# Optimization experiments

Hardware: AMD Instinct MI355X
Metric: run time of the kernel (lower is better)

The kernel has to match this reference:

```python
import jax, jax.numpy as jnp
import numpy as np

B, S, D, MD = 4, 4096, 1024, 512
SCALE = 0.02  # init scale for weights


def _layernorm(x, g, b, eps=1e-5):
    m = jnp.mean(x, axis=-1, keepdims=True)
    v = jnp.mean((x - m) ** 2, axis=-1, keepdims=True)
    return (x - m) * jax.lax.rsqrt(v + eps) * g + b


def _mem_mlp(h, W0, W1):
    # MemoryMLP depth=2: linear -> gelu -> linear (no biases)
    return jax.nn.gelu(h @ W0) @ W1


def _assoc_scan(gates, inputs):
    # state_t = g_t * state_{t-1} + in_t, over the seq axis (axis=1)
    def step(state, gi):
        g, i = gi
        s = g * state + i
        return s, s
    init = jnp.zeros_like(inputs[:, 0])
    _, out = jax.lax.scan(step, init, (jnp.moveaxis(gates, 1, 0), jnp.moveaxis(inputs, 1, 0)))
    return jnp.moveaxis(out, 1, 0)


def setup_inputs() -> dict:
    key = jax.random.key(0)
    ks = jax.random.split(key, 10)
    return {
        "x": jax.random.normal(ks[0], (B, S, D), jnp.float32),
        "Wd": jax.random.normal(ks[1], (D, MD), jnp.float32) * SCALE,
        "bd": jnp.zeros((MD,), jnp.float32),
        "Wu": jax.random.normal(ks[2], (MD, D), jnp.float32) * SCALE,
        "bu": jnp.zeros((D,), jnp.float32),
        "Wq": jax.random.normal(ks[3], (MD, MD), jnp.float32) * SCALE,
        "bq": jnp.zeros((MD,), jnp.float32),
        "Wk": jax.random.normal(ks[4], (MD, MD), jnp.float32) * SCALE,
        "bk": jnp.zeros((MD,), jnp.float32),
        "Wv": jax.random.normal(ks[5], (MD, MD), jnp.float32) * SCALE,
        "bv": jnp.zeros((MD,), jnp.float32),
        "q_gamma": jnp.ones((MD,), jnp.float32),
        "q_beta": jnp.zeros((MD,), jnp.float32),
        "k_gamma": jnp.ones((MD,), jnp.float32),
        "k_beta": jnp.zeros((MD,), jnp.float32),
        "W0": jax.random.normal(ks[6], (MD, MD), jnp.float32) * SCALE,
        "W1": jax.random.normal(ks[7], (MD, MD), jnp.float32) * SCALE,
        "adaptive_lr": jnp.full((1,), 0.01, jnp.float32),
        "forget_factor": jnp.full((1,), 0.1, jnp.float32),
    }


def reference(x, Wd, bd, Wu, bu, Wq, bq, Wk, bk, Wv, bv,
              q_gamma, q_beta, k_gamma, k_beta, W0, W1,
              adaptive_lr, forget_factor):
    h = x @ Wd + bd                                   # [B,S,MD] down_proj
    q = _layernorm(h @ Wq + bq, q_gamma, q_beta)      # q_norm(to_queries)
    k = _layernorm(h @ Wk + bk, k_gamma, k_beta)      # k_norm(to_keys)
    v = h @ Wv + bv                                   # to_values
    retrieved = _mem_mlp(q, W0, W1)                   # memory read
    pred = _mem_mlp(k, W0, W1)                        # memory store pred
    # per-token surprise: MSE over feature dim
    surprise = jnp.mean((pred - v) ** 2, axis=-1, keepdims=True)  # [B,S,1]
    gate_val = 1.0 - jax.nn.sigmoid(forget_factor)[0]
    gates = jnp.full((B, S, 1), 1.0, jnp.float32) * gate_val
    inputs = adaptive_lr[0] * surprise * v            # surprise-weighted write
    scanned = _assoc_scan(gates, inputs)              # sequential recurrence
    out = (retrieved + scanned) @ Wu + bu             # up_proj
    return out
```

## Files before the change

kernel.cpp:

```cpp
#include <hip/hip_runtime.h>
#include <hip/hip_bf16.h>
#include <math.h>

#define B_    4
#define S_    4096
#define DD    1024
#define MD    512
#define NTOK  16384
#define CHUNK 128
#define NCH   32

typedef unsigned short u16;
typedef __attribute__((ext_vector_type(8))) short short8;
typedef __attribute__((ext_vector_type(4))) float f32x4;

__device__ __forceinline__ float bf2f(u16 u) {
    unsigned int x = ((unsigned int)u) << 16;
    return __builtin_bit_cast(float, x);
}
__device__ __forceinline__ u16 f2bf(float f) {
    unsigned int x = __builtin_bit_cast(unsigned int, f);
    unsigned int lsb = (x >> 16) & 1u;
    x += 0x7fffu + lsb;
    return (u16)(x >> 16);
}
__device__ __forceinline__ float gelu_f(float x) {
    float x3 = x * x * x;
    return 0.5f * x * (1.0f + tanhf(0.7978845608028654f * (x + 0.044715f * x3)));
}
__device__ __forceinline__ float gate_from_ff(const float* ff) {
    return 1.0f - 1.0f / (1.0f + expf(-ff[0]));
}

#define GLDS(gp, lp) __builtin_amdgcn_global_load_lds( \
    (const __attribute__((address_space(1))) void*)(gp), \
    (__attribute__((address_space(3))) void*)(lp), 16, 0, 0)

template<int EPI, int HB, int OUTBF>
__global__ __launch_bounds__(256) void gemm_bf16_k(
    const u16* __restrict__ A, const u16* __restrict__ BT,
    const float* __restrict__ bias, void* __restrict__ C,
    int N, int K, int M)
{
    __shared__ __align__(16) u16 Al[2][128 * 32];
    __shared__ __align__(16) u16 Bl[2][128 * 32];
    const int tid = threadIdx.x;
    const int w = tid >> 6, l = tid & 63;
    const int rowBase = blockIdx.y * 128, colBase = blockIdx.x * 128;
    const int wm = (w >> 1) * 64, wn = (w & 1) * 64;

    const int srow = l >> 2;
    const int skoff = (l & 3) * 8;
    const u16* Ag0 = A  + (size_t)(rowBase + w * 16 + srow) * K + skoff;
    const u16* Ag1 = A  + (size_t)(rowBase + (w + 4) * 16 + srow) * K + skoff;
    const u16* Bg0 = BT + (size_t)(colBase + w * 16 + srow) * K + skoff;
    const u16* Bg1 = BT + (size_t)(colBase + (w + 4) * 16 + srow) * K + skoff;

    f32x4 acc[4][4];
#pragma unroll
    for (int i = 0; i < 4; ++i)
#pragma unroll
        for (int j = 0; j < 4; ++j) acc[i][j] = (f32x4){0.f, 0.f, 0.f, 0.f};

    const int KT = K >> 5;
    GLDS(Ag0, &Al[0][(w * 16) * 32]);
    GLDS(Ag1, &Al[0][((w + 4) * 16) * 32]);
    GLDS(Bg0, &Bl[0][(w * 16) * 32]);
    GLDS(Bg1, &Bl[0][((w + 4) * 16) * 32]);
    __syncthreads();

    const int lr = l & 15;
    const int goff = (l >> 4) * 8;
    int cur = 0;
    for (int kt = 0; kt < KT; ++kt) {
        if (kt + 1 < KT) {
            const size_t ko = (size_t)(kt + 1) << 5;
            GLDS(Ag0 + ko, &Al[cur ^ 1][(w * 16) * 32]);
            GLDS(Ag1 + ko, &Al[cur ^ 1][((w + 4) * 16) * 32]);
            GLDS(Bg0 + ko, &Bl[cur ^ 1][(w * 16) * 32]);
            GLDS(Bg1 + ko, &Bl[cur ^ 1][((w + 4) * 16) * 32]);
        }
        short8 af[4], bfr[4];
#pragma unroll
        for (int m = 0; m < 4; ++m)
            af[m] = *(const short8*)&Al[cur][(wm + m * 16 + lr) * 32 + goff];
#pragma unroll
        for (int n = 0; n < 4; ++n)
            bfr[n] = *(const short8*)&Bl[cur][(wn + n * 16 + lr) * 32 + goff];
#pragma unroll
        for (int m = 0; m < 4; ++m)
#pragma unroll
            for (int n = 0; n < 4; ++n)
                acc[m][n] = __builtin_amdgcn_mfma_f32_16x16x32_bf16(af[m], bfr[n], acc[m][n], 0, 0, 0);
        __syncthreads();
        cur ^= 1;
    }

    const int g4 = (l >> 4) * 4;
#pragma unroll
    for (int n = 0; n < 4; ++n) {
        const int col = colBase + wn + n * 16 + lr;
        const float bj = HB ? bias[col] : 0.0f;
#pragma unroll
        for (int m = 0; m < 4; ++m) {
            const int row0 = rowBase + wm + m * 16 + g4;
#pragma unroll
            for (int q = 0; q < 4; ++q) {
                float vv = acc[m][n][q] + bj;
                if (EPI == 1) vv = gelu_f(vv);
                if (OUTBF) ((u16*)C)[(size_t)(row0 + q) * M + col] = f2bf(vv);
                else       ((float*)C)[(size_t)(row0 + q) * M + col] = vv;
            }
        }
    }
}

__global__ __launch_bounds__(256) void cvt_bf16_k(const float* __restrict__ in,
                                                  u16* __restrict__ out, int n)
{
    size_t i = ((size_t)blockIdx.x * 256 + threadIdx.x) * 8;
    if (i + 8 > (size_t)n) return;
    float4 a = *(const float4*)(in + i);
    float4 b = *(const float4*)(in + i + 4);
    short8 o;
    o[0] = (short)f2bf(a.x); o[1] = (short)f2bf(a.y);
    o[2] = (short)f2bf(a.z); o[3] = (short)f2bf(a.w);
    o[4] = (short)f2bf(b.x); o[5] = (short)f2bf(b.y);
    o[6] = (short)f2bf(b.z); o[7] = (short)f2bf(b.w);
    *(short8*)(out + i) = o;
}

__global__ __launch_bounds__(256) void wtrans_k(const float* __restrict__ W,
                                                u16* __restrict__ WT, int K, int M)
{
    __shared__ float t[32][33];
    const int tx = threadIdx.x, ty = threadIdx.y;
    const int m0 = blockIdx.x * 32, k0 = blockIdx.y * 32;
#pragma unroll
    for (int i = 0; i < 4; ++i)
        t[ty + i * 8][tx] = W[(size_t)(k0 + ty + i * 8) * M + m0 + tx];
    __syncthreads();
#pragma unroll
    for (int i = 0; i < 4; ++i)
        WT[(size_t)(m0 + ty + i * 8) * K + k0 + tx] = f2bf(t[tx][ty + i * 8]);
}

__global__ __launch_bounds__(256) void wtrans5_k(
    const float* __restrict__ Wa, const float* __restrict__ Wb,
    const float* __restrict__ Wc, const float* __restrict__ Wd_,
    const float* __restrict__ We,
    u16* __restrict__ Ta, u16* __restrict__ Tb, u16* __restrict__ Tc,
    u16* __restrict__ Td, u16* __restrict__ Te)
{
    __shared__ float t[32][33];
    const float* W; u16* T;
    switch (blockIdx.z) {
        case 0: W = Wa; T = Ta; break;
        case 1: W = Wb; T = Tb; break;
        case 2: W = Wc; T = Tc; break;
        case 3: W = Wd_; T = Td; break;
        default: W = We; T = Te; break;
    }
    const int tx = threadIdx.x, ty = threadIdx.y;
    const int m0 = blockIdx.x * 32, k0 = blockIdx.y * 32;
#pragma unroll
    for (int i = 0; i < 4; ++i)
        t[ty + i * 8][tx] = W[(size_t)(k0 + ty + i * 8) * 512 + m0 + tx];
    __syncthreads();
#pragma unroll
    for (int i = 0; i < 4; ++i)
        T[(size_t)(m0 + ty + i * 8) * 512 + k0 + tx] = f2bf(t[tx][ty + i * 8]);
}

__global__ __launch_bounds__(256) void ln_k(const float* __restrict__ X,
                                            u16* __restrict__ Y,
                                            const float* __restrict__ g,
                                            const float* __restrict__ b)
{
    const int row = blockIdx.x, tid = threadIdx.x;
    const float* x = X + (size_t)row * MD;
    float v0 = x[tid], v1 = x[tid + 256];
    float s = v0 + v1, q = v0 * v0 + v1 * v1;
#pragma unroll
    for (int off = 32; off > 0; off >>= 1) {
        s += __shfl_down(s, off);
        q += __shfl_down(q, off);
    }
    __shared__ float redS[4], redQ[4];
    __shared__ float s_mean, s_rstd;
    const int lane = tid & 63, w = tid >> 6;
    if (lane == 0) { redS[w] = s; redQ[w] = q; }
    __syncthreads();
    if (tid == 0) {
        float S = redS[0] + redS[1] + redS[2] + redS[3];
        float Q = redQ[0] + redQ[1] + redQ[2] + redQ[3];
        float m = S * (1.f / 512.f);
        float var = Q * (1.f / 512.f) - m * m;
        s_mean = m; s_rstd = rsqrtf(var + 1e-5f);
    }
    __syncthreads();
    const float m = s_mean, rs = s_rstd;
    u16* y = Y + (size_t)row * MD;
    y[tid]       = f2bf((v0 - m) * rs * g[tid]       + b[tid]);
    y[tid + 256] = f2bf((v1 - m) * rs * g[tid + 256] + b[tid + 256]);
}

__global__ __launch_bounds__(256) void surprise_k(const u16* __restrict__ pred,
                                                  u16* __restrict__ v,
                                                  const float* __restrict__ lr_p)
{
    const int row = blockIdx.x, tid = threadIdx.x;
    const u16* pp = pred + (size_t)row * MD;
    u16* vp = v + (size_t)row * MD;
    float p0 = bf2f(pp[tid]), p1 = bf2f(pp[tid + 256]);
    float v0 = bf2f(vp[tid]), v1 = bf2f(vp[tid + 256]);
    float d0 = p0 - v0, d1 = p1 - v1;
    float q = d0 * d0 + d1 * d1;
#pragma unroll
    for (int off = 32; off > 0; off >>= 1) q += __shfl_down(q, off);
    __shared__ float redQ[4];
    __shared__ float s_coef;
    const int lane = tid & 63, w = tid >> 6;
    if (lane == 0) redQ[w] = q;
    __syncthreads();
    if (tid == 0) {
        float Q = redQ[0] + redQ[1] + redQ[2] + redQ[3];
        s_coef = lr_p[0] * (Q * (1.f / 512.f));
    }
    __syncthreads();
    const float c = s_coef;
    vp[tid]       = f2bf(c * v0);
    vp[tid + 256] = f2bf(c * v1);
}

__global__ __launch_bounds__(256) void scan1_k(u16* __restrict__ io,
                                               const float* __restrict__ ff,
                                               float* __restrict__ carry)
{
    const int idx = blockIdx.x * blockDim.x + threadIdx.x;
    const int d = idx & (MD - 1);
    const int c = (idx >> 9) & (NCH - 1);
    const int b = idx >> 14;
    const float g = gate_from_ff(ff);
    u16* p = io + ((size_t)(b * S_ + c * CHUNK)) * MD + d;
    float s = 0.f;
#pragma unroll 4
    for (int t = 0; t < CHUNK; ++t) {
        s = fmaf(g, s, bf2f(p[(size_t)t * MD]));
        p[(size_t)t * MD] = f2bf(s);
    }
    carry[((size_t)b * NCH + c) * MD + d] = s;
}

__global__ __launch_bounds__(256) void scan2_k(const float* __restrict__ carry,
                                               const float* __restrict__ ff,
                                               float* __restrict__ Sin)
{
    const int idx = blockIdx.x * blockDim.x + threadIdx.x;
    const int d = idx & (MD - 1);
    const int b = idx >> 9;
    const float g = gate_from_ff(ff);
    const float gL = powf(g, (float)CHUNK);
    float p = 0.f;
    for (int c = 0; c < NCH; ++c) {
        Sin[((size_t)b * NCH + c) * MD + d] = p;
        p = carry[((size_t)b * NCH + c) * MD + d] + gL * p;
    }
}

__global__ __launch_bounds__(256) void scan3_k(const u16* __restrict__ loc,
                                               const float* __restrict__ Sin,
                                               const float* __restrict__ retr,
                                               const float* __restrict__ ff,
                                               u16* __restrict__ fin)
{
    const size_t idx = (size_t)blockIdx.x * blockDim.x + threadIdx.x;
    const int d = (int)(idx & (MD - 1));
    const int t = (int)((idx >> 9) & (S_ - 1));
    const int b = (int)(idx >> 21);
    const int c = t >> 7, tl = t & (CHUNK - 1);
    const float g = gate_from_ff(ff);
    const float f = exp2f((float)(tl + 1) * log2f(g));
    float v = bf2f(loc[idx]) + f * Sin[((size_t)b * NCH + c) * MD + d] + retr[idx];
    fin[idx] = f2bf(v);
}

extern "C" void kernel_launch(void* const* d_in, const int* in_sizes, int n_in,
                              void* d_out, int out_size, void* d_ws, size_t ws_size,
                              hipStream_t stream) {
    const float* x   = (const float*)d_in[0];
    const float* Wd  = (const float*)d_in[1];
    const float* bd  = (const float*)d_in[2];
    const float* Wu  = (const float*)d_in[3];
    const float* bu  = (const float*)d_in[4];
    const float* Wq  = (const float*)d_in[5];
    const float* bq  = (const float*)d_in[6];
    const float* Wk  = (const float*)d_in[7];
    const float* bk  = (const float*)d_in[8];
    const float* Wv  = (const float*)d_in[9];
    const float* bv  = (const float*)d_in[10];
    const float* qg  = (const float*)d_in[11];
    const float* qb  = (const float*)d_in[12];
    const float* kg  = (const float*)d_in[13];
    const float* kb  = (const float*)d_in[14];
    const float* W0  = (const float*)d_in[15];
    const float* W1  = (const float*)d_in[16];
    const float* lr  = (const float*)d_in[17];
    const float* ff  = (const float*)d_in[18];
    float* out = (float*)d_out;

    u16* wdT = (u16*)d_ws;
    u16* wqT = wdT + 512 * 1024;
    u16* wkT = wqT + 512 * 512;
    u16* wvT = wkT + 512 * 512;
    u16* w0T = wvT + 512 * 512;
    u16* w1T = w0T + 512 * 512;
    u16* wuT = w1T + 512 * 512;
    u16* xb  = wuT + 1024 * 512;
    u16* b1  = xb;
    u16* b2  = xb + (size_t)NTOK * MD;
    u16* hb  = xb + (size_t)NTOK * DD;
    u16* b3  = hb;
    float* P   = (float*)(hb + (size_t)NTOK * MD);
    u16* VB    = (u16*)(P + (size_t)NTOK * MD);
    float* carry = (float*)(VB + (size_t)NTOK * MD);
    float* Sin   = carry + B_ * NCH * MD;

    dim3 blk(256);
    dim3 t32(32, 8);

    cvt_bf16_k<<<(NTOK * DD) / (256 * 8), blk, 0, stream>>>(x, xb, NTOK * DD);
    wtrans_k<<<dim3(512 / 32, 1024 / 32), t32, 0, stream>>>(Wd, wdT, 1024, 512);
    wtrans5_k<<<dim3(16, 16, 5), t32, 0, stream>>>(Wq, Wk, Wv, W0, W1,
                                                   wqT, wkT, wvT, w0T, w1T);
    wtrans_k<<<dim3(1024 / 32, 512 / 32), t32, 0, stream>>>(Wu, wuT, 512, 1024);

    gemm_bf16_k<0, 1, 1><<<dim3(4, 128), blk, 0, stream>>>(xb, wdT, bd, hb, NTOK, 1024, 512);
    gemm_bf16_k<0, 1, 0><<<dim3(4, 128), blk, 0, stream>>>(hb, wqT, bq, P, NTOK, 512, 512);
    ln_k<<<NTOK, blk, 0, stream>>>(P, b1, qg, qb);
    gemm_bf16_k<0, 1, 0><<<dim3(4, 128), blk, 0, stream>>>(hb, wkT, bk, P, NTOK, 512, 512);
    ln_k<<<NTOK, blk, 0, stream>>>(P, b2, kg, kb);
    gemm_bf16_k<0, 1, 1><<<dim3(4, 128), blk, 0, stream>>>(hb, wvT, bv, VB, NTOK, 512, 512);
    gemm_bf16_k<1, 0, 1><<<dim3(4, 128), blk, 0, stream>>>(b1, w0T, nullptr, b3, NTOK, 512, 512);
    gemm_bf16_k<0, 0, 0><<<dim3(4, 128), blk, 0, stream>>>(b3, w1T, nullptr, P, NTOK, 512, 512);
    gemm_bf16_k<1, 0, 1><<<dim3(4, 128), blk, 0, stream>>>(b2, w0T, nullptr, b3, NTOK, 512, 512);
    gemm_bf16_k<0, 0, 1><<<dim3(4, 128), blk, 0, stream>>>(b3, w1T, nullptr, b1, NTOK, 512, 512);
    surprise_k<<<NTOK, blk, 0, stream>>>(b1, VB, lr);
    scan1_k<<<(B_ * NCH * MD) / 256, blk, 0, stream>>>(VB, ff, carry);
    scan2_k<<<(B_ * MD) / 256, blk, 0, stream>>>(carry, ff, Sin);
    scan3_k<<<(NTOK * MD) / 256, blk, 0, stream>>>(VB, Sin, P, ff, b2);
    gemm_bf16_k<0, 1, 0><<<dim3(8, 128), blk, 0, stream>>>(b2, wuT, bu, out, NTOK, 512, 1024);
}
```

Before: 304.5 us.

## Fuse QKV projections and batch memory-MLP GEMMs; vectorize scan and packed bf16 stores

Concatenates Wq/Wk/Wv into one GEMM that writes bf16 outputs into three segmented buffers, and runs LayerNorm for q and k in place in a single launch. The two memory-MLP passes share one GEMM pair over 2*NTOK rows (q and k buffers are contiguous). The surprise coefficient is folded into the scan instead of rewriting V, scan kernels use 4-wide vector loads with smaller chunks, and the GEMM epilogue packs bf16 pairs via lane shuffles. The down-projection uses a narrower 64-column tile for more blocks. This reduces launches and intermediate fp32 round trips at the cost of more template complexity and bf16 rounding of pre-LN activations.

```diff
diff --git a/kernel.cpp b/kernel.cpp
--- a/kernel.cpp
+++ b/kernel.cpp
@@ -7,20 +7,22 @@
 #define DD    1024
 #define MD    512
 #define NTOK  16384
-#define CHUNK 128
-#define NCH   32
+#define CHUNK 32
+#define NCH   128
 
 typedef unsigned short u16;
+typedef unsigned int u32;
 typedef __attribute__((ext_vector_type(8))) short short8;
 typedef __attribute__((ext_vector_type(4))) float f32x4;
+typedef __attribute__((ext_vector_type(4))) unsigned short us4;
 
 __device__ __forceinline__ float bf2f(u16 u) {
-    unsigned int x = ((unsigned int)u) << 16;
+    u32 x = ((u32)u) << 16;
     return __builtin_bit_cast(float, x);
 }
 __device__ __forceinline__ u16 f2bf(float f) {
-    unsigned int x = __builtin_bit_cast(unsigned int, f);
-    unsigned int lsb = (x >> 16) & 1u;
+    u32 x = __builtin_bit_cast(u32, f);
+    u32 lsb = (x >> 16) & 1u;
     x += 0x7fffu + lsb;
     return (u16)(x >> 16);
 }
@@ -36,37 +38,40 @@
     (const __attribute__((address_space(1))) void*)(gp), \
     (__attribute__((address_space(3))) void*)(lp), 16, 0, 0)
 
-template<int EPI, int HB, int OUTBF>
+template<int NF, int EPI, int HB, int OUTBF, int SEG>
 __global__ __launch_bounds__(256) void gemm_bf16_k(
     const u16* __restrict__ A, const u16* __restrict__ BT,
-    const float* __restrict__ bias, void* __restrict__ C,
-    int N, int K, int M)
-{
+    const float* __restrict__ bias0, const float* __restrict__ bias1,
+    const float* __restrict__ bias2,
+    void* __restrict__ out0, void* __restrict__ out1, void* __restrict__ out2,
+    int N, int K, int M, int OM)
+{
+    constexpr int TN = 32 * NF;
     __shared__ __align__(16) u16 Al[2][128 * 32];
-    __shared__ __align__(16) u16 Bl[2][128 * 32];
+    __shared__ __align__(16) u16 Bl[2][TN * 32];
     const int tid = threadIdx.x;
     const int w = tid >> 6, l = tid & 63;
-    const int rowBase = blockIdx.y * 128, colBase = blockIdx.x * 128;
-    const int wm = (w >> 1) * 64, wn = (w & 1) * 64;
+    const int rowBase = blockIdx.y * 128, colBase = blockIdx.x * TN;
+    const int wm = (w >> 1) * 64, wn = (w & 1) * 16 * NF;
 
     const int srow = l >> 2;
     const int skoff = (l & 3) * 8;
-    const u16* Ag0 = A  + (size_t)(rowBase + w * 16 + srow) * K + skoff;
-    const u16* Ag1 = A  + (size_t)(rowBase + (w + 4) * 16 + srow) * K + skoff;
+    const u16* Ag0 = A + (size_t)(rowBase + w * 16 + srow) * K + skoff;
+    const u16* Ag1 = A + (size_t)(rowBase + (w + 4) * 16 + srow) * K + skoff;
     const u16* Bg0 = BT + (size_t)(colBase + w * 16 + srow) * K + skoff;
-    const u16* Bg1 = BT + (size_t)(colBase + (w + 4) * 16 + srow) * K + skoff;
-
-    f32x4 acc[4][4];
-#pragma unroll
-    for (int i = 0; i < 4; ++i)
-#pragma unroll
-        for (int j = 0; j < 4; ++j) acc[i][j] = (f32x4){0.f, 0.f, 0.f, 0.f};
+    const u16* Bg1 = (NF == 4) ? BT + (size_t)(colBase + (w + 4) * 16 + srow) * K + skoff : nullptr;
+
+    f32x4 acc[4][NF];
+#pragma unroll
+    for (int i = 0; i < 4; ++i)
+#pragma unroll
+        for (int j = 0; j < NF; ++j) acc[i][j] = (f32x4){0.f, 0.f, 0.f, 0.f};
 
     const int KT = K >> 5;
     GLDS(Ag0, &Al[0][(w * 16) * 32]);
     GLDS(Ag1, &Al[0][((w + 4) * 16) * 32]);
     GLDS(Bg0, &Bl[0][(w * 16) * 32]);
-    GLDS(Bg1, &Bl[0][((w + 4) * 16) * 32]);
+    if (NF == 4) GLDS(Bg1, &Bl[0][((w + 4) * 16) * 32]);
     __syncthreads();
 
     const int lr = l & 15;
@@ -78,38 +83,62 @@
             GLDS(Ag0 + ko, &Al[cur ^ 1][(w * 16) * 32]);
             GLDS(Ag1 + ko, &Al[cur ^ 1][((w + 4) * 16) * 32]);
             GLDS(Bg0 + ko, &Bl[cur ^ 1][(w * 16) * 32]);
-            GLDS(Bg1 + ko, &Bl[cur ^ 1][((w + 4) * 16) * 32]);
+            if (NF == 4) GLDS(Bg1 + ko, &Bl[cur ^ 1][((w + 4) * 16) * 32]);
         }
-        short8 af[4], bfr[4];
+        short8 af[4], bfr[NF];
 #pragma unroll
         for (int m = 0; m < 4; ++m)
             af[m] = *(const short8*)&Al[cur][(wm + m * 16 + lr) * 32 + goff];
 #pragma unroll
-        for (int n = 0; n < 4; ++n)
+        for (int n = 0; n < NF; ++n)
             bfr[n] = *(const short8*)&Bl[cur][(wn + n * 16 + lr) * 32 + goff];
 #pragma unroll
         for (int m = 0; m < 4; ++m)
 #pragma unroll
-            for (int n = 0; n < 4; ++n)
+            for (int n = 0; n < NF; ++n)
                 acc[m][n] = __builtin_amdgcn_mfma_f32_16x16x32_bf16(af[m], bfr[n], acc[m][n], 0, 0, 0);
         __syncthreads();
         cur ^= 1;
     }
 
     const int g4 = (l >> 4) * 4;
-#pragma unroll
-    for (int n = 0; n < 4; ++n) {
+    const bool odd = l & 1;
+#pragma unroll
+    for (int n = 0; n < NF; ++n) {
         const int col = colBase + wn + n * 16 + lr;
-        const float bj = HB ? bias[col] : 0.0f;
+        const int seg = SEG ? (col >> 9) : 0;
+        const int lcol = SEG ? (col - (seg << 9)) : col;
+        const float* bp = (seg == 0) ? bias0 : (seg == 1) ? bias1 : bias2;
+        void* outp = (seg == 0) ? out0 : (seg == 1) ? out1 : out2;
+        const float bj = HB ? bp[lcol] : 0.0f;
 #pragma unroll
         for (int m = 0; m < 4; ++m) {
             const int row0 = rowBase + wm + m * 16 + g4;
+            float vq[4];
 #pragma unroll
             for (int q = 0; q < 4; ++q) {
                 float vv = acc[m][n][q] + bj;
                 if (EPI == 1) vv = gelu_f(vv);
-                if (OUTBF) ((u16*)C)[(size_t)(row0 + q) * M + col] = f2bf(vv);
-                else       ((float*)C)[(size_t)(row0 + q) * M + col] = vv;
+                vq[q] = vv;
+            }
+            if (OUTBF) {
+                float pv[4];
+#pragma unroll
+                for (int q = 0; q < 4; ++q) pv[q] = __shfl_xor(vq[q], 1);
+                const int q0 = odd ? 2 : 0;
+                u16* ob = (u16*)outp;
+#pragma unroll
+                for (int j = 0; j < 2; ++j) {
+                    const int qq = q0 + j;
+                    float lo = odd ? pv[qq] : vq[qq];
+                    float hi = odd ? vq[qq] : pv[qq];
+                    u32 word = (u32)f2bf(lo) | ((u32)f2bf(hi) << 16);
+                    *(u32*)(ob + (size_t)(row0 + qq) * OM + (lcol & ~1)) = word;
+                }
+            } else {
+#pragma unroll
+                for (int q = 0; q < 4; ++q)
+                    ((float*)outp)[(size_t)(row0 + q) * OM + lcol] = vq[q];
             }
         }
     }
@@ -172,14 +201,15 @@
         T[(size_t)(m0 + ty + i * 8) * 512 + k0 + tx] = f2bf(t[tx][ty + i * 8]);
 }
 
-__global__ __launch_bounds__(256) void ln_k(const float* __restrict__ X,
-                                            u16* __restrict__ Y,
-                                            const float* __restrict__ g,
-                                            const float* __restrict__ b)
+__global__ __launch_bounds__(256) void ln2_k(u16* __restrict__ X0, u16* __restrict__ X1,
+                                             const float* __restrict__ g0, const float* __restrict__ b0,
+                                             const float* __restrict__ g1, const float* __restrict__ b1)
 {
     const int row = blockIdx.x, tid = threadIdx.x;
-    const float* x = X + (size_t)row * MD;
-    float v0 = x[tid], v1 = x[tid + 256];
+    u16* x = (blockIdx.y ? X1 : X0) + (size_t)row * MD;
+    const float* g = blockIdx.y ? g1 : g0;
+    const float* b = blockIdx.y ? b1 : b0;
+    float v0 = bf2f(x[tid]), v1 = bf2f(x[tid + 256]);
     float s = v0 + v1, q = v0 * v0 + v1 * v1;
 #pragma unroll
     for (int off = 32; off > 0; off >>= 1) {
@@ -200,56 +230,60 @@
     }
     __syncthreads();
     const float m = s_mean, rs = s_rstd;
-    u16* y = Y + (size_t)row * MD;
-    y[tid]       = f2bf((v0 - m) * rs * g[tid]       + b[tid]);
-    y[tid + 256] = f2bf((v1 - m) * rs * g[tid + 256] + b[tid + 256]);
+    x[tid]       = f2bf((v0 - m) * rs * g[tid]       + b[tid]);
+    x[tid + 256] = f2bf((v1 - m) * rs * g[tid + 256] + b[tid + 256]);
 }
 
 __global__ __launch_bounds__(256) void surprise_k(const u16* __restrict__ pred,
-                                                  u16* __restrict__ v,
-                                                  const float* __restrict__ lr_p)
+                                                  const u16* __restrict__ v,
+                                                  const float* __restrict__ lr_p,
+                                                  float* __restrict__ coef)
 {
     const int row = blockIdx.x, tid = threadIdx.x;
     const u16* pp = pred + (size_t)row * MD;
-    u16* vp = v + (size_t)row * MD;
-    float p0 = bf2f(pp[tid]), p1 = bf2f(pp[tid + 256]);
-    float v0 = bf2f(vp[tid]), v1 = bf2f(vp[tid + 256]);
-    float d0 = p0 - v0, d1 = p1 - v1;
+    const u16* vp = v + (size_t)row * MD;
+    float d0 = bf2f(pp[tid]) - bf2f(vp[tid]);
+    float d1 = bf2f(pp[tid + 256]) - bf2f(vp[tid + 256]);
     float q = d0 * d0 + d1 * d1;
 #pragma unroll
     for (int off = 32; off > 0; off >>= 1) q += __shfl_down(q, off);
     __shared__ float redQ[4];
-    __shared__ float s_coef;
     const int lane = tid & 63, w = tid >> 6;
     if (lane == 0) redQ[w] = q;
     __syncthreads();
     if (tid == 0) {
         float Q = redQ[0] + redQ[1] + redQ[2] + redQ[3];
-        s_coef = lr_p[0] * (Q * (1.f / 512.f));
-    }
-    __syncthreads();
-    const float c = s_coef;
-    vp[tid]       = f2bf(c * v0);
-    vp[tid + 256] = f2bf(c * v1);
+        coef[row] = lr_p[0] * (Q * (1.f / 512.f));
+    }
 }
 
 __global__ __launch_bounds__(256) void scan1_k(u16* __restrict__ io,
+                                               const float* __restrict__ coef,
                                                const float* __restrict__ ff,
                                                float* __restrict__ carry)
 {
     const int idx = blockIdx.x * blockDim.x + threadIdx.x;
-    const int d = idx & (MD - 1);
-    const int c = (idx >> 9) & (NCH - 1);
+    const int d4 = (idx & 127) * 4;
+    const int c = (idx >> 7) & (NCH - 1);
     const int b = idx >> 14;
     const float g = gate_from_ff(ff);
-    u16* p = io + ((size_t)(b * S_ + c * CHUNK)) * MD + d;
-    float s = 0.f;
+    const int tok0 = b * S_ + c * CHUNK;
+    u16* p = io + (size_t)tok0 * MD + d4;
+    const float* cf = coef + tok0;
+    float s0 = 0.f, s1 = 0.f, s2 = 0.f, s3 = 0.f;
 #pragma unroll 4
     for (int t = 0; t < CHUNK; ++t) {
-        s = fmaf(g, s, bf2f(p[(size_t)t * MD]));
-        p[(size_t)t * MD] = f2bf(s);
-    }
-    carry[((size_t)b * NCH + c) * MD + d] = s;
+        us4 vv = *(const us4*)(p + (size_t)t * MD);
+        const float ct = cf[t];
+        s0 = fmaf(g, s0, ct * bf2f(vv.x));
+        s1 = fmaf(g, s1, ct * bf2f(vv.y));
+        s2 = fmaf(g, s2, ct * bf2f(vv.z));
+        s3 = fmaf(g, s3, ct * bf2f(vv.w));
+        us4 ov = { f2bf(s0), f2bf(s1), f2bf(s2), f2bf(s3) };
+        *(us4*)(p + (size_t)t * MD) = ov;
+    }
+    float4 cw = { s0, s1, s2, s3 };
+    *(float4*)(carry + ((size_t)b * NCH + c) * MD + d4) = cw;
 }
 
 __global__ __launch_bounds__(256) void scan2_k(const float* __restrict__ carry,
@@ -270,19 +304,27 @@
 
 __global__ __launch_bounds__(256) void scan3_k(const u16* __restrict__ loc,
                                                const float* __restrict__ Sin,
-                                               const float* __restrict__ retr,
+                                               const u16* __restrict__ retr,
                                                const float* __restrict__ ff,
                                                u16* __restrict__ fin)
 {
     const size_t idx = (size_t)blockIdx.x * blockDim.x + threadIdx.x;
-    const int d = (int)(idx & (MD - 1));
-    const int t = (int)((idx >> 9) & (S_ - 1));
-    const int b = (int)(idx >> 21);
-    const int c = t >> 7, tl = t & (CHUNK - 1);
+    const int d4 = (int)(idx & 127) * 4;
+    const int t = (int)((idx >> 7) & (S_ - 1));
+    const int b = (int)(idx >> 19);
+    const int c = t >> 5, tl = t & (CHUNK - 1);
     const float g = gate_from_ff(ff);
     const float f = exp2f((float)(tl + 1) * log2f(g));
-    float v = bf2f(loc[idx]) + f * Sin[((size_t)b * NCH + c) * MD + d] + retr[idx];
-    fin[idx] = f2bf(v);
+    const size_t row = (size_t)(b * S_ + t) * MD + d4;
+    us4 lv = *(const us4*)(loc + row);
+    us4 rv = *(const us4*)(retr + row);
+    float4 sv = *(const float4*)(Sin + ((size_t)b * NCH + c) * MD + d4);
+    us4 ov;
+    ov.x = f2bf(bf2f(lv.x) + f * sv.x + bf2f(rv.x));
+    ov.y = f2bf(bf2f(lv.y) + f * sv.y + bf2f(rv.y));
+    ov.z = f2bf(bf2f(lv.z) + f * sv.z + bf2f(rv.z));
+    ov.w = f2bf(bf2f(lv.w) + f * sv.w + bf2f(rv.w));
+    *(us4*)(fin + row) = ov;
 }
 
 extern "C" void kernel_launch(void* const* d_in, const int* in_sizes, int n_in,
@@ -309,45 +351,42 @@
     const float* ff  = (const float*)d_in[18];
     float* out = (float*)d_out;
 
-    u16* wdT = (u16*)d_ws;
-    u16* wqT = wdT + 512 * 1024;
-    u16* wkT = wqT + 512 * 512;
-    u16* wvT = wkT + 512 * 512;
-    u16* w0T = wvT + 512 * 512;
-    u16* w1T = w0T + 512 * 512;
-    u16* wuT = w1T + 512 * 512;
-    u16* xb  = wuT + 1024 * 512;
-    u16* b1  = xb;
-    u16* b2  = xb + (size_t)NTOK * MD;
-    u16* hb  = xb + (size_t)NTOK * DD;
-    u16* b3  = hb;
-    float* P   = (float*)(hb + (size_t)NTOK * MD);
-    u16* VB    = (u16*)(P + (size_t)NTOK * MD);
-    float* carry = (float*)(VB + (size_t)NTOK * MD);
-    float* Sin   = carry + B_ * NCH * MD;
+    u16* wdT   = (u16*)d_ws;
+    u16* wqkvT = wdT + 512 * 1024;
+    u16* w0T   = wqkvT + 1536 * 512;
+    u16* w1T   = w0T + 512 * 512;
+    u16* wuT   = w1T + 512 * 512;
+    u16* xb    = wuT + 1024 * 512;
+    u16* hb    = xb + (size_t)NTOK * DD;
+    u16* b1    = hb + (size_t)NTOK * MD;
+    u16* b2    = b1 + (size_t)NTOK * MD;
+    u16* VB    = b2 + (size_t)NTOK * MD;
+    float* coef  = (float*)(VB + (size_t)NTOK * MD);
+    float* carry = coef + NTOK;
+    float* Sin   = carry + (size_t)B_ * NCH * MD;
 
     dim3 blk(256);
     dim3 t32(32, 8);
 
     cvt_bf16_k<<<(NTOK * DD) / (256 * 8), blk, 0, stream>>>(x, xb, NTOK * DD);
-    wtrans_k<<<dim3(512 / 32, 1024 / 32), t32, 0, stream>>>(Wd, wdT, 1024, 512);
+    wtrans_k<<<dim3(16, 32), t32, 0, stream>>>(Wd, wdT, 1024, 512);
     wtrans5_k<<<dim3(16, 16, 5), t32, 0, stream>>>(Wq, Wk, Wv, W0, W1,
-                                                   wqT, wkT, wvT, w0T, w1T);
-    wtrans_k<<<dim3(1024 / 32, 512 / 32), t32, 0, stream>>>(Wu, wuT, 512, 1024);
-
-    gemm_bf16_k<0, 1, 1><<<dim3(4, 128), blk, 0, stream>>>(xb, wdT, bd, hb, NTOK, 1024, 512);
-    gemm_bf16_k<0, 1, 0><<<dim3(4, 128), blk, 0, stream>>>(hb, wqT, bq, P, NTOK, 512, 512);
-    ln_k<<<NTOK, blk, 0, stream>>>(P, b1, qg, qb);
-    gemm_bf16_k<0, 1, 0><<<dim3(4, 128), blk, 0, stream>>>(hb, wkT, bk, P, NTOK, 512, 512);
-    ln_k<<<NTOK, blk, 0, stream>>>(P, b2, kg, kb);
-    gemm_bf16_k<0, 1, 1><<<dim3(4, 128), blk, 0, stream>>>(hb, wvT, bv, VB, NTOK, 512, 512);
-    gemm_bf16_k<1, 0, 1><<<dim3(4, 128), blk, 0, stream>>>(b1, w0T, nullptr, b3, NTOK, 512, 512);
-    gemm_bf16_k<0, 0, 0><<<dim3(4, 128), blk, 0, stream>>>(b3, w1T, nullptr, P, NTOK, 512, 512);
-    gemm_bf16_k<1, 0, 1><<<dim3(4, 128), blk, 0, stream>>>(b2, w0T, nullptr, b3, NTOK, 512, 512);
-    gemm_bf16_k<0, 0, 1><<<dim3(4, 128), blk, 0, stream>>>(b3, w1T, nullptr, b1, NTOK, 512, 512);
-    surprise_k<<<NTOK, blk, 0, stream>>>(b1, VB, lr);
-    scan1_k<<<(B_ * NCH * MD) / 256, blk, 0, stream>>>(VB, ff, carry);
+        wqkvT, wqkvT + 512 * 512, wqkvT + 2 * 512 * 512, w0T, w1T);
+    wtrans_k<<<dim3(32, 16), t32, 0, stream>>>(Wu, wuT, 512, 1024);
+
+    gemm_bf16_k<2, 0, 1, 1, 0><<<dim3(8, 128), blk, 0, stream>>>(
+        xb, wdT, bd, bd, bd, hb, hb, hb, NTOK, 1024, 512, 512);
+    gemm_bf16_k<4, 0, 1, 1, 1><<<dim3(12, 128), blk, 0, stream>>>(
+        hb, wqkvT, bq, bk, bv, b1, b2, VB, NTOK, 512, 1536, 512);
+    ln2_k<<<dim3(NTOK, 2), blk, 0, stream>>>(b1, b2, qg, qb, kg, kb);
+    gemm_bf16_k<4, 1, 0, 1, 0><<<dim3(4, 256), blk, 0, stream>>>(
+        b1, w0T, nullptr, nullptr, nullptr, xb, xb, xb, 2 * NTOK, 512, 512, 512);
+    gemm_bf16_k<4, 0, 0, 1, 0><<<dim3(4, 256), blk, 0, stream>>>(
+        xb, w1T, nullptr, nullptr, nullptr, b1, b1, b1, 2 * NTOK, 512, 512, 512);
+    surprise_k<<<NTOK, blk, 0, stream>>>(b2, VB, lr, coef);
+    scan1_k<<<(B_ * NCH * (MD / 4)) / 256, blk, 0, stream>>>(VB, coef, ff, carry);
     scan2_k<<<(B_ * MD) / 256, blk, 0, stream>>>(carry, ff, Sin);
-    scan3_k<<<(NTOK * MD) / 256, blk, 0, stream>>>(VB, Sin, P, ff, b2);
-    gemm_bf16_k<0, 1, 0><<<dim3(8, 128), blk, 0, stream>>>(b2, wuT, bu, out, NTOK, 512, 1024);
-}
+    scan3_k<<<(NTOK * (MD / 4)) / 256, blk, 0, stream>>>(VB, Sin, b1, ff, b2);
+    gemm_bf16_k<4, 0, 1, 0, 0><<<dim3(8, 128), blk, 0, stream>>>(
+        b2, wuT, bu, bu, bu, out, out, out, NTOK, 512, 1024, 1024);
+}
```

Result: slower. 360.7 us (+18.5%).
